# Performance work log

Measured on AMD Instinct MI355X. Metric: run time of the kernel, lower is better.

## Reference

```python
import jax, jax.numpy as jnp
import numpy as np

# Faithful Bilinear layer (bilin_axis=0, 3D inputs [L, B, D]).
# Original TF code builds the full [L,B,L,B] tensordot then extracts the
# diagonal over the B axes; mathematically the result is
#   out[b, l, m] = tensor0[l, b, :] @ kernel @ tensor1[m, b, :] + bias
# which we compute directly with one einsum (same math, no redundant B^2 work).

L, B, D = 4096, 4, 64


def setup_inputs() -> dict:
    key = jax.random.key(0)
    k0, k1, k2 = jax.random.split(key, 3)
    tensor0 = jax.random.normal(k0, (L, B, D), dtype=jnp.float32)
    tensor1 = jax.random.normal(k1, (L, B, D), dtype=jnp.float32)
    kernel = jax.random.normal(k2, (D, D), dtype=jnp.float32) * (1.0 / np.sqrt(D))
    bias = jnp.zeros((1,), dtype=jnp.float32)  # scalar bias, broadcasts
    return {"tensor0": tensor0, "tensor1": tensor1, "kernel": kernel, "bias": bias}


def reference(tensor0, tensor1, kernel, bias):
    # Q_tensor1[m,b,d] = sum_e tensor1[m,b,e] * kernel[d,e]  (tensordot axes [-1],[1])
    # then contract tensor0 over d and keep only the b-diagonal -> [B, L, L]
    out = jnp.einsum("lbd,de,mbe->blm", tensor0, kernel, tensor1)
    out = out + bias[0]          # scalar bias
    return out[None]              # expand_dims(0) -> [1, B, L, L]
```

## Files before the change

kernel.cpp:

```cpp
#include <hip/hip_runtime.h>
#include <hip/hip_bf16.h>

#define LDIM 4096
#define BDIM 4
#define DDIM 64

typedef __attribute__((ext_vector_type(4))) float f32x4;
typedef __attribute__((ext_vector_type(8))) __bf16 bf16x8;

__device__ __forceinline__ bf16x8 cvt8(f32x4 a, f32x4 b) {
    bf16x8 r;
    r[0] = (__bf16)a[0]; r[1] = (__bf16)a[1]; r[2] = (__bf16)a[2]; r[3] = (__bf16)a[3];
    r[4] = (__bf16)b[0]; r[5] = (__bf16)b[1]; r[6] = (__bf16)b[2]; r[7] = (__bf16)b[3];
    return r;
}

__device__ __forceinline__ void gload_lds16(const void* g, void* l) {
    __builtin_amdgcn_global_load_lds(
        (const __attribute__((address_space(1))) void*)g,
        (__attribute__((address_space(3))) void*)l, 16, 0, 0);
}

__global__ __launch_bounds__(256) void prep_kernel(
    const float* __restrict__ t0,
    const float* __restrict__ t1,
    const float* __restrict__ kmat,
    __hip_bfloat16* __restrict__ Abf,
    __hip_bfloat16* __restrict__ Qbf)
{
    const int tid  = threadIdx.x;
    const int w    = tid >> 6;
    const int lane = tid & 63;
    const int lr   = lane & 15;
    const int lhi  = lane >> 4;
    const int rbase = blockIdx.x * 64 + w * 16;

    f32x4 acc[4] = {{0.f,0.f,0.f,0.f},{0.f,0.f,0.f,0.f},{0.f,0.f,0.f,0.f},{0.f,0.f,0.f,0.f}};
#pragma unroll
    for (int ks = 0; ks < 2; ++ks) {
        const float* ap = t1 + (size_t)(rbase + lr) * DDIM + ks * 32 + lhi * 8;
        bf16x8 af = cvt8(*(const f32x4*)ap, *(const f32x4*)(ap + 4));
#pragma unroll
        for (int nt = 0; nt < 4; ++nt) {
            const float* bp = kmat + (size_t)(nt * 16 + lr) * DDIM + ks * 32 + lhi * 8;
            bf16x8 bq = cvt8(*(const f32x4*)bp, *(const f32x4*)(bp + 4));
            acc[nt] = __builtin_amdgcn_mfma_f32_16x16x32_bf16(af, bq, acc[nt], 0, 0, 0);
        }
    }
#pragma unroll
    for (int nt = 0; nt < 4; ++nt) {
#pragma unroll
        for (int j = 0; j < 4; ++j) {
            const int r = rbase + lhi * 4 + j;
            const int m = r >> 2, b = r & 3;
            Qbf[((size_t)(b * LDIM) + m) * DDIM + nt * 16 + lr] =
                __float2bfloat16(acc[nt][j]);
        }
    }

    {
        const int r2 = blockIdx.x * 64 + (tid >> 2);
        const int d0 = (tid & 3) * 16;
        const float* src = t0 + (size_t)r2 * DDIM + d0;
        f32x4 v0 = *(const f32x4*)(src + 0);
        f32x4 v1 = *(const f32x4*)(src + 4);
        f32x4 v2 = *(const f32x4*)(src + 8);
        f32x4 v3 = *(const f32x4*)(src + 12);
        const int m2 = r2 >> 2, b2 = r2 & 3;
        __hip_bfloat16* dst = Abf + ((size_t)(b2 * LDIM) + m2) * DDIM + d0;
        *(bf16x8*)dst       = cvt8(v0, v1);
        *(bf16x8*)(dst + 8) = cvt8(v2, v3);
    }
}

__global__ __launch_bounds__(512, 4) void gemm_kernel(
    const __hip_bfloat16* __restrict__ Abf,
    const __hip_bfloat16* __restrict__ Qbf,
    const float* __restrict__ bias,
    float* __restrict__ out)
{
    __shared__ char smem[49152];

    const int bid0 = blockIdx.x;
    const int swz  = (bid0 & 7) * 256 + (bid0 >> 3);
    const int b    = swz >> 9;
    const int t    = swz & 511;
    const int tr   = t >> 4;
    const int tc   = t & 15;

    const int tid  = threadIdx.x;
    const int w    = tid >> 6;
    const int lane = tid & 63;
    const int wr   = w >> 2, wc = w & 3;
    const int lr   = lane & 15;
    const int lhi  = lane >> 4;

    const char* Apan = (const char*)(Abf + ((size_t)b * LDIM + tr * 128) * DDIM);
    const char* Bpan = (const char*)(Qbf + ((size_t)b * LDIM + tc * 256) * DDIM);

#pragma unroll
    for (int i = 0; i < 2; ++i) {
        const int ci  = i * 8 + w;
        const int row = ci * 8 + (lane >> 3);
        const int so  = row * 128 + (((lane & 7) ^ (row & 7)) << 4);
        gload_lds16(Apan + so, smem + ci * 1024);
    }
#pragma unroll
    for (int i = 0; i < 4; ++i) {
        const int ci  = i * 8 + w;
        const int row = ci * 8 + (lane >> 3);
        const int so  = row * 128 + (((lane & 7) ^ (row & 7)) << 4);
        gload_lds16(Bpan + so, smem + 16384 + ci * 1024);
    }
    __syncthreads();

    const char* As = smem;
    const char* Bs = smem + 16384;

    f32x4 acc[4][4] = {};
#pragma unroll
    for (int ks = 0; ks < 2; ++ks) {
        const int kx = ks * 4 + lhi;
        bf16x8 af[4], bq[4];
#pragma unroll
        for (int mi = 0; mi < 4; ++mi) {
            const int row = wr * 64 + mi * 16 + lr;
            af[mi] = *(const bf16x8*)(As + row * 128 + ((kx ^ (lr & 7)) << 4));
        }
#pragma unroll
        for (int ni = 0; ni < 4; ++ni) {
            const int row = wc * 64 + ni * 16 + lr;
            bq[ni] = *(const bf16x8*)(Bs + row * 128 + ((kx ^ (lr & 7)) << 4));
        }
#pragma unroll
        for (int mi = 0; mi < 4; ++mi)
#pragma unroll
            for (int ni = 0; ni < 4; ++ni)
                acc[mi][ni] = __builtin_amdgcn_mfma_f32_16x16x32_bf16(
                    af[mi], bq[ni], acc[mi][ni], 0, 0, 0);
    }

    const float bs = bias[0];
    float* outp = out + (size_t)b * LDIM * LDIM;
    const int rowb = tr * 128 + wr * 64;
    const int colb = tc * 256 + wc * 64;
#pragma unroll
    for (int mi = 0; mi < 4; ++mi) {
#pragma unroll
        for (int ni = 0; ni < 4; ++ni) {
            const int col = colb + ni * 16 + lr;
#pragma unroll
            for (int j = 0; j < 4; ++j) {
                const int row = rowb + mi * 16 + lhi * 4 + j;
                outp[(size_t)row * LDIM + col] = acc[mi][ni][j] + bs;
            }
        }
    }
}

extern "C" void kernel_launch(void* const* d_in, const int* in_sizes, int n_in,
                              void* d_out, int out_size, void* d_ws, size_t ws_size,
                              hipStream_t stream) {
    const float* t0   = (const float*)d_in[0];
    const float* t1   = (const float*)d_in[1];
    const float* km   = (const float*)d_in[2];
    const float* bias = (const float*)d_in[3];
    float* out = (float*)d_out;

    __hip_bfloat16* Abf = (__hip_bfloat16*)d_ws;
    __hip_bfloat16* Qbf = Abf + (size_t)BDIM * LDIM * DDIM;

    prep_kernel<<<256, 256, 0, stream>>>(t0, t1, km, Abf, Qbf);
    gemm_kernel<<<2048, 512, 0, stream>>>(Abf, Qbf, bias, out);
}
```

Before: 53.99 us.

## Fuse projection and bf16 conversion into the GEMM kernel, dropping prep pass

```diff
diff --git a/kernel.cpp b/kernel.cpp
--- a/kernel.cpp
+++ b/kernel.cpp
@@ -7,6 +7,7 @@
 
 typedef __attribute__((ext_vector_type(4))) float f32x4;
 typedef __attribute__((ext_vector_type(8))) __bf16 bf16x8;
+typedef __attribute__((ext_vector_type(4))) __bf16 bf16x4;
 
 __device__ __forceinline__ bf16x8 cvt8(f32x4 a, f32x4 b) {
     bf16x8 r;
@@ -15,67 +16,10 @@
     return r;
 }
 
-__device__ __forceinline__ void gload_lds16(const void* g, void* l) {
-    __builtin_amdgcn_global_load_lds(
-        (const __attribute__((address_space(1))) void*)g,
-        (__attribute__((address_space(3))) void*)l, 16, 0, 0);
-}
-
-__global__ __launch_bounds__(256) void prep_kernel(
+__global__ __launch_bounds__(512, 4) void fused_kernel(
     const float* __restrict__ t0,
     const float* __restrict__ t1,
     const float* __restrict__ kmat,
-    __hip_bfloat16* __restrict__ Abf,
-    __hip_bfloat16* __restrict__ Qbf)
-{
-    const int tid  = threadIdx.x;
-    const int w    = tid >> 6;
-    const int lane = tid & 63;
-    const int lr   = lane & 15;
-    const int lhi  = lane >> 4;
-    const int rbase = blockIdx.x * 64 + w * 16;
-
-    f32x4 acc[4] = {{0.f,0.f,0.f,0.f},{0.f,0.f,0.f,0.f},{0.f,0.f,0.f,0.f},{0.f,0.f,0.f,0.f}};
-#pragma unroll
-    for (int ks = 0; ks < 2; ++ks) {
-        const float* ap = t1 + (size_t)(rbase + lr) * DDIM + ks * 32 + lhi * 8;
-        bf16x8 af = cvt8(*(const f32x4*)ap, *(const f32x4*)(ap + 4));
-#pragma unroll
-        for (int nt = 0; nt < 4; ++nt) {
-            const float* bp = kmat + (size_t)(nt * 16 + lr) * DDIM + ks * 32 + lhi * 8;
-            bf16x8 bq = cvt8(*(const f32x4*)bp, *(const f32x4*)(bp + 4));
-            acc[nt] = __builtin_amdgcn_mfma_f32_16x16x32_bf16(af, bq, acc[nt], 0, 0, 0);
-        }
-    }
-#pragma unroll
-    for (int nt = 0; nt < 4; ++nt) {
-#pragma unroll
-        for (int j = 0; j < 4; ++j) {
-            const int r = rbase + lhi * 4 + j;
-            const int m = r >> 2, b = r & 3;
-            Qbf[((size_t)(b * LDIM) + m) * DDIM + nt * 16 + lr] =
-                __float2bfloat16(acc[nt][j]);
-        }
-    }
-
-    {
-        const int r2 = blockIdx.x * 64 + (tid >> 2);
-        const int d0 = (tid & 3) * 16;
-        const float* src = t0 + (size_t)r2 * DDIM + d0;
-        f32x4 v0 = *(const f32x4*)(src + 0);
-        f32x4 v1 = *(const f32x4*)(src + 4);
-        f32x4 v2 = *(const f32x4*)(src + 8);
-        f32x4 v3 = *(const f32x4*)(src + 12);
-        const int m2 = r2 >> 2, b2 = r2 & 3;
-        __hip_bfloat16* dst = Abf + ((size_t)(b2 * LDIM) + m2) * DDIM + d0;
-        *(bf16x8*)dst       = cvt8(v0, v1);
-        *(bf16x8*)(dst + 8) = cvt8(v2, v3);
-    }
-}
-
-__global__ __launch_bounds__(512, 4) void gemm_kernel(
-    const __hip_bfloat16* __restrict__ Abf,
-    const __hip_bfloat16* __restrict__ Qbf,
     const float* __restrict__ bias,
     float* __restrict__ out)
 {
@@ -95,27 +39,65 @@
     const int lr   = lane & 15;
     const int lhi  = lane >> 4;
 
-    const char* Apan = (const char*)(Abf + ((size_t)b * LDIM + tr * 128) * DDIM);
-    const char* Bpan = (const char*)(Qbf + ((size_t)b * LDIM + tc * 256) * DDIM);
+    char* As = smem;
+    char* Bs = smem + 16384;
+
+    {
+        bf16x8 ka[4][2];
+#pragma unroll
+        for (int dt = 0; dt < 4; ++dt)
+#pragma unroll
+            for (int ks = 0; ks < 2; ++ks) {
+                const float* kp = kmat + (size_t)(dt * 16 + lr) * DDIM + ks * 32 + lhi * 8;
+                ka[dt][ks] = cvt8(*(const f32x4*)kp, *(const f32x4*)(kp + 4));
+            }
+        bf16x8 tb[2][2];
+#pragma unroll
+        for (int mt = 0; mt < 2; ++mt) {
+            const int mloc = w * 32 + mt * 16 + lr;
+            const float* tp = t1 + ((size_t)(tc * 256 + mloc) * BDIM + b) * DDIM;
+#pragma unroll
+            for (int ks = 0; ks < 2; ++ks)
+                tb[mt][ks] = cvt8(*(const f32x4*)(tp + ks * 32 + lhi * 8),
+                                  *(const f32x4*)(tp + ks * 32 + lhi * 8 + 4));
+        }
+        f32x4 qacc[4][2] = {};
+#pragma unroll
+        for (int ks = 0; ks < 2; ++ks)
+#pragma unroll
+            for (int dt = 0; dt < 4; ++dt)
+#pragma unroll
+                for (int mt = 0; mt < 2; ++mt)
+                    qacc[dt][mt] = __builtin_amdgcn_mfma_f32_16x16x32_bf16(
+                        ka[dt][ks], tb[mt][ks], qacc[dt][mt], 0, 0, 0);
 
 #pragma unroll
-    for (int i = 0; i < 2; ++i) {
-        const int ci  = i * 8 + w;
-        const int row = ci * 8 + (lane >> 3);
-        const int so  = row * 128 + (((lane & 7) ^ (row & 7)) << 4);
-        gload_lds16(Apan + so, smem + ci * 1024);
+        for (int dt = 0; dt < 4; ++dt)
+#pragma unroll
+            for (int mt = 0; mt < 2; ++mt) {
+                const int mloc = w * 32 + mt * 16 + lr;
+                const int ch   = (dt * 2 + (lhi >> 1)) ^ (mloc & 7);
+                bf16x4 qv;
+                qv[0] = (__bf16)qacc[dt][mt][0];
+                qv[1] = (__bf16)qacc[dt][mt][1];
+                qv[2] = (__bf16)qacc[dt][mt][2];
+                qv[3] = (__bf16)qacc[dt][mt][3];
+                *(bf16x4*)(Bs + mloc * 128 + (ch << 4) + (lhi & 1) * 8) = qv;
+            }
     }
-#pragma unroll
-    for (int i = 0; i < 4; ++i) {
-        const int ci  = i * 8 + w;
-        const int row = ci * 8 + (lane >> 3);
-        const int so  = row * 128 + (((lane & 7) ^ (row & 7)) << 4);
-        gload_lds16(Bpan + so, smem + 16384 + ci * 1024);
+
+    {
+        const int r  = tid >> 2;
+        const int cj = (tid & 3) * 2;
+        const float* sp = t0 + ((size_t)(tr * 128 + r) * BDIM + b) * DDIM + cj * 8;
+        f32x4 a0 = *(const f32x4*)(sp + 0);
+        f32x4 a1 = *(const f32x4*)(sp + 4);
+        f32x4 a2 = *(const f32x4*)(sp + 8);
+        f32x4 a3 = *(const f32x4*)(sp + 12);
+        *(bf16x8*)(As + r * 128 + ((cj ^ (r & 7)) << 4))       = cvt8(a0, a1);
+        *(bf16x8*)(As + r * 128 + (((cj + 1) ^ (r & 7)) << 4)) = cvt8(a2, a3);
     }
     __syncthreads();
-
-    const char* As = smem;
-    const char* Bs = smem + 16384;
 
     f32x4 acc[4][4] = {};
 #pragma unroll
@@ -167,9 +149,5 @@
     const float* bias = (const float*)d_in[3];
     float* out = (float*)d_out;
 
-    __hip_bfloat16* Abf = (__hip_bfloat16*)d_ws;
-    __hip_bfloat16* Qbf = Abf + (size_t)BDIM * LDIM * DDIM;
-
-    prep_kernel<<<256, 256, 0, stream>>>(t0, t1, km, Abf, Qbf);
-    gemm_kernel<<<2048, 512, 0, stream>>>(Abf, Qbf, bias, out);
+    fused_kernel<<<2048, 512, 0, stream>>>(t0, t1, km, bias, out);
 }
```

New measurement: 78.43 us. 1.45x slower.
